# Optimization experiments

Hardware: AMD Instinct MI355X
Metric: run time of the kernel (lower is better)

Reference implementation:

```python
import jax, jax.numpy as jnp
import numpy as np

NEG_SLOPE = 0.2
EPS = 1e-16


def gat_conv(x, src, dst, W, a_src, a_dst, bias, heads, out_ch, n_nodes):
    # x: [N, in], W: [in, heads*out_ch], a_src/a_dst: [heads, out_ch]
    h = (x @ W).reshape(n_nodes, heads, out_ch)            # [N,H,C]
    s_src = jnp.sum(h * a_src[None], axis=-1)              # [N,H]
    s_dst = jnp.sum(h * a_dst[None], axis=-1)              # [N,H]
    e = jax.nn.leaky_relu(s_src[src] + s_dst[dst], NEG_SLOPE)  # [E,H]
    # segment softmax over incoming edges of each destination node
    m = jax.ops.segment_max(e, dst, num_segments=n_nodes)  # [N,H]
    e = jnp.exp(e - m[dst])
    z = jax.ops.segment_sum(e, dst, num_segments=n_nodes)  # [N,H]
    alpha = e / (z[dst] + EPS)                             # [E,H]
    msg = h[src] * alpha[:, :, None]                       # [E,H,C]
    out = jax.ops.segment_sum(msg, dst, num_segments=n_nodes)
    return out.reshape(n_nodes, heads * out_ch) + bias


def setup_inputs() -> dict:
    key = jax.random.key(0)
    ks = jax.random.split(key, 12)
    N, E, D_IN, HID, HEADS, OUT = 100000, 1600000, 16, 128, 8, 3
    C1 = HID // HEADS  # 16 per head
    glorot = lambda k, shape: jax.random.normal(k, shape, jnp.float32) * np.sqrt(2.0 / (shape[0] + shape[-1]))
    return {
        "feature": jax.random.normal(ks[0], (N, D_IN), jnp.float32),
        "edge_index": jax.random.randint(ks[1], (2, E), 0, N, jnp.int64),
        "edge_type": jax.random.randint(ks[2], (E,), 0, 2, jnp.int64),
        "W1": glorot(ks[3], (D_IN, HEADS * C1)),
        "a_src1": glorot(ks[4], (HEADS, C1)),
        "a_dst1": glorot(ks[5], (HEADS, C1)),
        "b1": jnp.zeros((HID,), jnp.float32),
        "W2": glorot(ks[6], (HID, OUT)),
        "a_src2": glorot(ks[7], (1, OUT)),
        "a_dst2": glorot(ks[8], (1, OUT)),
        "b2": jnp.zeros((OUT,), jnp.float32),
    }


def reference(feature, edge_index, edge_type, W1, a_src1, a_dst1, b1, W2, a_src2, a_dst2, b2):
    N = feature.shape[0]
    # PyG GATConv adds self-loops by default
    loop = jnp.arange(N, dtype=edge_index.dtype)
    src = jnp.concatenate([edge_index[0], loop])
    dst = jnp.concatenate([edge_index[1], loop])
    x = gat_conv(feature, src, dst, W1, a_src1, a_dst1, b1, heads=8, out_ch=16, n_nodes=N)
    x = jax.nn.relu(x)
    # dropout is identity in eval mode
    x = gat_conv(x, src, dst, W2, a_src2, a_dst2, b2, heads=1, out_ch=3, n_nodes=N)
    return x
```

## Files before the change

### kernel.cpp

```cpp
#include <hip/hip_runtime.h>
#include <hip/hip_bf16.h>
#include <hip/hip_fp16.h>
#include <math.h>

#define NEG_SLOPE 0.2f
#define GAT_EPS 1e-16f
#define NBMAX 512
#define CAP   6144

__global__ __launch_bounds__(1024) void k_partA(
    const int* __restrict__ ei, int E, int N, int NB, int G2,
    int* __restrict__ cnt, unsigned int* __restrict__ bp,
    const float* __restrict__ x, const float* __restrict__ W1,
    const float* __restrict__ a_src, const float* __restrict__ a_dst,
    __half* __restrict__ h1, float* __restrict__ s_src, float* __restrict__ s_dst)
{
    __shared__ int hist[NBMAX];
    __shared__ int base[NBMAX];
    int t = threadIdx.x;
    if (blockIdx.x >= G2) {
        int gid = (blockIdx.x - G2) * 1024 + t;
        int n = gid >> 5;
        int j4 = gid & 31;
        if (n >= N) return;
        const float4* xr = (const float4*)(x + (size_t)n * 16);
        float4 x0 = xr[0], x1 = xr[1], x2 = xr[2], x3 = xr[3];
        float xs[16] = { x0.x,x0.y,x0.z,x0.w, x1.x,x1.y,x1.z,x1.w,
                         x2.x,x2.y,x2.z,x2.w, x3.x,x3.y,x3.z,x3.w };
        const float4* W4 = (const float4*)W1;
        float4 acc = {0.f, 0.f, 0.f, 0.f};
#pragma unroll
        for (int k = 0; k < 16; ++k) {
            float4 w = W4[k * 32 + j4];
            acc.x += xs[k] * w.x;
            acc.y += xs[k] * w.y;
            acc.z += xs[k] * w.z;
            acc.w += xs[k] * w.w;
        }
        union { __half2 h2v[2]; uint2 u; } pk;
        pk.h2v[0] = __floats2half2_rn(acc.x, acc.y);
        pk.h2v[1] = __floats2half2_rn(acc.z, acc.w);
        ((uint2*)h1)[(size_t)n * 32 + j4] = pk.u;
        float4 av = ((const float4*)a_src)[j4];
        float4 dv = ((const float4*)a_dst)[j4];
        float ps = acc.x*av.x + acc.y*av.y + acc.z*av.z + acc.w*av.w;
        float pd = acc.x*dv.x + acc.y*dv.y + acc.z*dv.z + acc.w*dv.w;
        ps += __shfl_xor(ps, 1); ps += __shfl_xor(ps, 2);
        pd += __shfl_xor(pd, 1); pd += __shfl_xor(pd, 2);
        if ((j4 & 3) == 0) {
            int h = j4 >> 2;
            s_src[n * 8 + h] = ps;
            s_dst[n * 8 + h] = pd;
        }
        return;
    }
    int e0 = blockIdx.x * 4096;
    int srcs[4], dsts[4];
#pragma unroll
    for (int k = 0; k < 4; ++k) {
        int e = e0 + k * 1024 + t;
        if (e < E + N) {
            if (e < E) { srcs[k] = ei[e]; dsts[k] = ei[E + e]; }
            else       { srcs[k] = dsts[k] = e - E; }
        } else dsts[k] = -1;
    }
    if (t < NB) hist[t] = 0;
    __syncthreads();
#pragma unroll
    for (int k = 0; k < 4; ++k)
        if (dsts[k] >= 0) atomicAdd(&hist[dsts[k] >> 8], 1);
    __syncthreads();
    if (t < NB) {
        int c = hist[t];
        base[t] = (c > 0) ? atomicAdd(&cnt[t], c) : 0;
        hist[t] = 0;
    }
    __syncthreads();
#pragma unroll
    for (int k = 0; k < 4; ++k) {
        if (dsts[k] >= 0) {
            int b = dsts[k] >> 8;
            int r = base[b] + atomicAdd(&hist[b], 1);
            if (r < CAP)
                bp[(size_t)b * CAP + r] =
                    ((unsigned)(dsts[k] & 255) << 17) | (unsigned)srcs[k];
        }
    }
}

__global__ __launch_bounds__(512) void k_csr(
    const unsigned int* __restrict__ bp, const int* __restrict__ cnt,
    int* __restrict__ offs, int* __restrict__ ends,
    int* __restrict__ csr, int N)
{
    __shared__ int dcount[256];
    __shared__ int dtmp[256];
    __shared__ int doff[256];
    int b = blockIdx.x;
    int t = threadIdx.x;
    int rb = b * CAP;
    int m = cnt[b]; if (m > CAP) m = CAP;
    if (t < 256) dcount[t] = 0;
    __syncthreads();
    for (int i = t; i < m; i += 512) {
        atomicAdd(&dcount[bp[rb + i] >> 17], 1);
    }
    __syncthreads();
    int v = 0;
    if (t < 256) { v = dcount[t]; dtmp[t] = v; }
    __syncthreads();
    for (int off = 1; off < 256; off <<= 1) {
        int add = (t < 256 && t >= off) ? dtmp[t - off] : 0;
        __syncthreads();
        if (t < 256) dtmp[t] += add;
        __syncthreads();
    }
    if (t < 256) {
        doff[t] = dtmp[t] - v;
        int n = b * 256 + t;
        if (n < N) { offs[n] = rb + doff[t]; ends[n] = rb + dtmp[t]; }
        dcount[t] = 0;
    }
    __syncthreads();
    for (int i = t; i < m; i += 512) {
        unsigned int p = bp[rb + i];
        int dl = p >> 17;
        int r = atomicAdd(&dcount[dl], 1);
        csr[rb + doff[dl] + r] = (int)(p & 0x1FFFFu);
    }
}

__global__ __launch_bounds__(256) void k_agg1(
    const __half* __restrict__ h1, const float* __restrict__ s_src,
    const float* __restrict__ s_dst, const float* __restrict__ b1,
    const float* __restrict__ W2, const float* __restrict__ a_src2,
    const float* __restrict__ a_dst2,
    const int* __restrict__ offs, const int* __restrict__ ends,
    const int* __restrict__ csr_src,
    float4* __restrict__ h2packed, float* __restrict__ s2d, int N)
{
    int gid = blockIdx.x * 256 + threadIdx.x;
    if (gid >= N * 16) return;
    int n = gid >> 4;
    int t = gid & 15;
    int h = t & 7;
    int half = t >> 3;
    int beg = offs[n], end = ends[n];
    float sd = s_dst[n * 8 + h];

    float z = 0.f;
    float acc[16];
#pragma unroll
    for (int c = 0; c < 16; ++c) acc[c] = 0.f;

    union U { float4 f; __half2 hh[4]; };
    int i = beg + half;
    for (; i + 2 < end; i += 4) {
        int sA = csr_src[i];
        int sB = csr_src[i + 2];
        const float4* hA = (const float4*)(h1 + (size_t)sA * 128 + h * 16);
        const float4* hB = (const float4*)(h1 + (size_t)sB * 128 + h * 16);
        U a0, a1, b0, b1v;
        a0.f = hA[0]; a1.f = hA[1];
        b0.f = hB[0]; b1v.f = hB[1];
        float eA = s_src[sA * 8 + h] + sd;
        float eB = s_src[sB * 8 + h] + sd;
        eA = (eA > 0.f) ? eA : NEG_SLOPE * eA;
        eB = (eB > 0.f) ? eB : NEG_SLOPE * eB;
        float pA = __expf(eA);
        float pB = __expf(eB);
        z += pA + pB;
#pragma unroll
        for (int k = 0; k < 4; ++k) {
            float2 vA = __half22float2(a0.hh[k]);
            float2 vB = __half22float2(b0.hh[k]);
            acc[2 * k]     += pA * vA.x + pB * vB.x;
            acc[2 * k + 1] += pA * vA.y + pB * vB.y;
        }
#pragma unroll
        for (int k = 0; k < 4; ++k) {
            float2 vA = __half22float2(a1.hh[k]);
            float2 vB = __half22float2(b1v.hh[k]);
            acc[8 + 2 * k] += pA * vA.x + pB * vB.x;
            acc[9 + 2 * k] += pA * vA.y + pB * vB.y;
        }
    }
    if (i < end) {
        int sA = csr_src[i];
        const float4* hA = (const float4*)(h1 + (size_t)sA * 128 + h * 16);
        U a0, a1;
        a0.f = hA[0]; a1.f = hA[1];
        float eA = s_src[sA * 8 + h] + sd;
        eA = (eA > 0.f) ? eA : NEG_SLOPE * eA;
        float pA = __expf(eA);
        z += pA;
#pragma unroll
        for (int k = 0; k < 4; ++k) {
            float2 vA = __half22float2(a0.hh[k]);
            acc[2 * k]     += pA * vA.x;
            acc[2 * k + 1] += pA * vA.y;
        }
#pragma unroll
        for (int k = 0; k < 4; ++k) {
            float2 vA = __half22float2(a1.hh[k]);
            acc[8 + 2 * k] += pA * vA.x;
            acc[9 + 2 * k] += pA * vA.y;
        }
    }

    z += __shfl_xor(z, 8);
#pragma unroll
    for (int c = 0; c < 16; ++c) acc[c] += __shfl_xor(acc[c], 8);

    float inv = 1.f / (z + GAT_EPS);

    float r0 = 0.f, r1 = 0.f, r2 = 0.f;
    const float* bb = b1 + h * 16;
    const float* w2 = W2 + h * 16 * 3;
#pragma unroll
    for (int c = 0; c < 16; ++c) {
        float xc = fmaxf(acc[c] * inv + bb[c], 0.f);
        r0 += xc * w2[c * 3 + 0];
        r1 += xc * w2[c * 3 + 1];
        r2 += xc * w2[c * 3 + 2];
    }
#pragma unroll
    for (int m = 4; m >= 1; m >>= 1) {
        r0 += __shfl_xor(r0, m);
        r1 += __shfl_xor(r1, m);
        r2 += __shfl_xor(r2, m);
    }
    if (t == 0) {
        float ss = r0 * a_src2[0] + r1 * a_src2[1] + r2 * a_src2[2];
        float dd = r0 * a_dst2[0] + r1 * a_dst2[1] + r2 * a_dst2[2];
        float4 pk = { r0, r1, r2, ss };
        h2packed[n] = pk;
        s2d[n] = dd;
    }
}

__global__ __launch_bounds__(256) void k_agg2(
    const float4* __restrict__ h2packed, const float* __restrict__ s2d,
    const float* __restrict__ b2,
    const int* __restrict__ offs, const int* __restrict__ ends,
    const int* __restrict__ csr_src,
    float* __restrict__ out, int N)
{
    int gid = blockIdx.x * 256 + threadIdx.x;
    if (gid >= N * 8) return;
    int n = gid >> 3;
    int t = gid & 7;
    int beg = offs[n], end = ends[n];
    float sd = s2d[n];
    float z = 0.f, a0 = 0.f, a1 = 0.f, a2 = 0.f;
    for (int i = beg + t; i < end; i += 8) {
        int src = csr_src[i];
        float4 v = h2packed[src];
        float s = v.w + sd;
        s = (s > 0.f) ? s : NEG_SLOPE * s;
        float p = __expf(s);
        z += p;
        a0 += p * v.x; a1 += p * v.y; a2 += p * v.z;
    }
#pragma unroll
    for (int m = 4; m >= 1; m >>= 1) {
        z  += __shfl_xor(z, m);
        a0 += __shfl_xor(a0, m);
        a1 += __shfl_xor(a1, m);
        a2 += __shfl_xor(a2, m);
    }
    if (t == 0) {
        float inv = 1.f / (z + GAT_EPS);
        out[(size_t)n * 3 + 0] = a0 * inv + b2[0];
        out[(size_t)n * 3 + 1] = a1 * inv + b2[1];
        out[(size_t)n * 3 + 2] = a2 * inv + b2[2];
    }
}

extern "C" void kernel_launch(void* const* d_in, const int* in_sizes, int n_in,
                              void* d_out, int out_size, void* d_ws, size_t ws_size,
                              hipStream_t stream)
{
    const float* feature = (const float*)d_in[0];
    const int*   ei      = (const int*)d_in[1];
    const float* W1      = (const float*)d_in[3];
    const float* a_src1  = (const float*)d_in[4];
    const float* a_dst1  = (const float*)d_in[5];
    const float* b1      = (const float*)d_in[6];
    const float* W2      = (const float*)d_in[7];
    const float* a_src2  = (const float*)d_in[8];
    const float* a_dst2  = (const float*)d_in[9];
    const float* b2      = (const float*)d_in[10];

    const int N = in_sizes[0] / 16;
    const int E = in_sizes[1] / 2;
    const int ET = E + N;
    const int NB = (N + 255) >> 8;

    char* p = (char*)d_ws;
    auto alloc = [&](size_t bytes) -> void* {
        void* r = (void*)p;
        p += (bytes + 255) & ~(size_t)255;
        return r;
    };
    __half* h1   = (__half*)alloc((size_t)N * 128 * 2);
    float*  s1s  = (float*)alloc((size_t)N * 8 * 4);
    float*  s1d  = (float*)alloc((size_t)N * 8 * 4);
    float4* h2pk = (float4*)alloc((size_t)N * 16);
    float*  s2dv = (float*)alloc((size_t)N * 4);
    int*    offs = (int*)alloc((size_t)N * 4);
    int*    ends = (int*)alloc((size_t)N * 4);
    int*    csr  = (int*)alloc((size_t)NB * CAP * 4);
    unsigned int* bp = (unsigned int*)alloc((size_t)NB * CAP * 4);
    int*    cnt  = (int*)alloc((size_t)NBMAX * 4);

    hipMemsetAsync(cnt, 0, (size_t)NB * 4, stream);

    int G2 = (ET + 4095) / 4096;
    int G1 = (N * 32 + 1023) / 1024;
    k_partA<<<G2 + G1, 1024, 0, stream>>>(
        ei, E, N, NB, G2, cnt, bp,
        feature, W1, a_src1, a_dst1, h1, s1s, s1d);

    k_csr<<<NB, 512, 0, stream>>>(bp, cnt, offs, ends, csr, N);

    k_agg1<<<(N * 16 + 255) / 256, 256, 0, stream>>>(
        h1, s1s, s1d, b1, W2, a_src2, a_dst2, offs, ends, csr, h2pk, s2dv, N);

    k_agg2<<<(N * 8 + 255) / 256, 256, 0, stream>>>(
        h2pk, s2dv, b2, offs, ends, csr, (float*)d_out, N);
}
```

Before: 172.9 us.

## Store layer-1 features head-major and aggregate one head per block

Layer-1 projected features and attention scores are now stored head-major ([H][N][C]) instead of node-major, and the first aggregation kernel assigns each block a single head over 128 destination nodes. Each block's gathers then touch one 3.2 MB head slice, which is meant to improve L2 locality for the random source gathers. Because the per-node reduction across heads can no longer happen inside a wavefront, per-head partial projections are written to a new N×8 float4 buffer and summed by an extra k_score2 kernel. This adds an extra launch and roughly 12.8 MB of extra write and read traffic.

After: 293.7 us. 1.7x slower.

```diff
diff --git a/kernel.cpp b/kernel.cpp
--- a/kernel.cpp
+++ b/kernel.cpp
@@ -13,7 +13,7 @@
     int* __restrict__ cnt, unsigned int* __restrict__ bp,
     const float* __restrict__ x, const float* __restrict__ W1,
     const float* __restrict__ a_src, const float* __restrict__ a_dst,
-    __half* __restrict__ h1, float* __restrict__ s_src, float* __restrict__ s_dst)
+    __half* __restrict__ h1h, float* __restrict__ s_src_h, float* __restrict__ s_dst_h)
 {
     __shared__ int hist[NBMAX];
     __shared__ int base[NBMAX];
@@ -37,20 +37,20 @@
             acc.z += xs[k] * w.z;
             acc.w += xs[k] * w.w;
         }
+        int h = j4 >> 2, c4 = j4 & 3;
         union { __half2 h2v[2]; uint2 u; } pk;
         pk.h2v[0] = __floats2half2_rn(acc.x, acc.y);
         pk.h2v[1] = __floats2half2_rn(acc.z, acc.w);
-        ((uint2*)h1)[(size_t)n * 32 + j4] = pk.u;
+        ((uint2*)h1h)[((size_t)h * N + n) * 4 + c4] = pk.u;
         float4 av = ((const float4*)a_src)[j4];
         float4 dv = ((const float4*)a_dst)[j4];
         float ps = acc.x*av.x + acc.y*av.y + acc.z*av.z + acc.w*av.w;
         float pd = acc.x*dv.x + acc.y*dv.y + acc.z*dv.z + acc.w*dv.w;
         ps += __shfl_xor(ps, 1); ps += __shfl_xor(ps, 2);
         pd += __shfl_xor(pd, 1); pd += __shfl_xor(pd, 2);
-        if ((j4 & 3) == 0) {
-            int h = j4 >> 2;
-            s_src[n * 8 + h] = ps;
-            s_dst[n * 8 + h] = pd;
+        if (c4 == 0) {
+            s_src_h[(size_t)h * N + n] = ps;
+            s_dst_h[(size_t)h * N + n] = pd;
         }
         return;
     }
@@ -130,23 +130,24 @@
     }
 }
 
-__global__ __launch_bounds__(256) void k_agg1(
-    const __half* __restrict__ h1, const float* __restrict__ s_src,
-    const float* __restrict__ s_dst, const float* __restrict__ b1,
-    const float* __restrict__ W2, const float* __restrict__ a_src2,
-    const float* __restrict__ a_dst2,
+__global__ __launch_bounds__(256) void k_agg1h(
+    const __half* __restrict__ h1h, const float* __restrict__ s_src_h,
+    const float* __restrict__ s_dst_h, const float* __restrict__ b1,
+    const float* __restrict__ W2,
     const int* __restrict__ offs, const int* __restrict__ ends,
     const int* __restrict__ csr_src,
-    float4* __restrict__ h2packed, float* __restrict__ s2d, int N)
-{
-    int gid = blockIdx.x * 256 + threadIdx.x;
-    if (gid >= N * 16) return;
-    int n = gid >> 4;
-    int t = gid & 15;
-    int h = t & 7;
-    int half = t >> 3;
+    float4* __restrict__ h2part, int N)
+{
+    int h = blockIdx.x & 7;
+    int chunk = blockIdx.x >> 3;
+    int t = threadIdx.x;
+    int n = chunk * 128 + (t >> 1);
+    int half = t & 1;
+    if (n >= N) return;
     int beg = offs[n], end = ends[n];
-    float sd = s_dst[n * 8 + h];
+    const float* ssrc = s_src_h + (size_t)h * N;
+    const __half* hbase = h1h + (size_t)h * N * 16;
+    float sd = s_dst_h[(size_t)h * N + n];
 
     float z = 0.f;
     float acc[16];
@@ -158,13 +159,13 @@
     for (; i + 2 < end; i += 4) {
         int sA = csr_src[i];
         int sB = csr_src[i + 2];
-        const float4* hA = (const float4*)(h1 + (size_t)sA * 128 + h * 16);
-        const float4* hB = (const float4*)(h1 + (size_t)sB * 128 + h * 16);
+        const float4* hA = (const float4*)(hbase + (size_t)sA * 16);
+        const float4* hB = (const float4*)(hbase + (size_t)sB * 16);
         U a0, a1, b0, b1v;
         a0.f = hA[0]; a1.f = hA[1];
         b0.f = hB[0]; b1v.f = hB[1];
-        float eA = s_src[sA * 8 + h] + sd;
-        float eB = s_src[sB * 8 + h] + sd;
+        float eA = ssrc[sA] + sd;
+        float eB = ssrc[sB] + sd;
         eA = (eA > 0.f) ? eA : NEG_SLOPE * eA;
         eB = (eB > 0.f) ? eB : NEG_SLOPE * eB;
         float pA = __expf(eA);
@@ -187,10 +188,10 @@
     }
     if (i < end) {
         int sA = csr_src[i];
-        const float4* hA = (const float4*)(h1 + (size_t)sA * 128 + h * 16);
+        const float4* hA = (const float4*)(hbase + (size_t)sA * 16);
         U a0, a1;
         a0.f = hA[0]; a1.f = hA[1];
-        float eA = s_src[sA * 8 + h] + sd;
+        float eA = ssrc[sA] + sd;
         eA = (eA > 0.f) ? eA : NEG_SLOPE * eA;
         float pA = __expf(eA);
         z += pA;
@@ -208,35 +209,45 @@
         }
     }
 
-    z += __shfl_xor(z, 8);
-#pragma unroll
-    for (int c = 0; c < 16; ++c) acc[c] += __shfl_xor(acc[c], 8);
-
-    float inv = 1.f / (z + GAT_EPS);
-
+    z += __shfl_xor(z, 1);
+#pragma unroll
+    for (int c = 0; c < 16; ++c) acc[c] += __shfl_xor(acc[c], 1);
+
+    if (half == 0) {
+        float inv = 1.f / (z + GAT_EPS);
+        float r0 = 0.f, r1 = 0.f, r2 = 0.f;
+        const float* bb = b1 + h * 16;
+        const float* w2 = W2 + h * 16 * 3;
+#pragma unroll
+        for (int c = 0; c < 16; ++c) {
+            float xc = fmaxf(acc[c] * inv + bb[c], 0.f);
+            r0 += xc * w2[c * 3 + 0];
+            r1 += xc * w2[c * 3 + 1];
+            r2 += xc * w2[c * 3 + 2];
+        }
+        float4 pk = { r0, r1, r2, 0.f };
+        h2part[(size_t)h * N + n] = pk;
+    }
+}
+
+__global__ __launch_bounds__(256) void k_score2(
+    const float4* __restrict__ h2part, const float* __restrict__ a_src2,
+    const float* __restrict__ a_dst2,
+    float4* __restrict__ h2pk, float* __restrict__ s2d, int N)
+{
+    int n = blockIdx.x * 256 + threadIdx.x;
+    if (n >= N) return;
     float r0 = 0.f, r1 = 0.f, r2 = 0.f;
-    const float* bb = b1 + h * 16;
-    const float* w2 = W2 + h * 16 * 3;
-#pragma unroll
-    for (int c = 0; c < 16; ++c) {
-        float xc = fmaxf(acc[c] * inv + bb[c], 0.f);
-        r0 += xc * w2[c * 3 + 0];
-        r1 += xc * w2[c * 3 + 1];
-        r2 += xc * w2[c * 3 + 2];
-    }
-#pragma unroll
-    for (int m = 4; m >= 1; m >>= 1) {
-        r0 += __shfl_xor(r0, m);
-        r1 += __shfl_xor(r1, m);
-        r2 += __shfl_xor(r2, m);
-    }
-    if (t == 0) {
-        float ss = r0 * a_src2[0] + r1 * a_src2[1] + r2 * a_src2[2];
-        float dd = r0 * a_dst2[0] + r1 * a_dst2[1] + r2 * a_dst2[2];
-        float4 pk = { r0, r1, r2, ss };
-        h2packed[n] = pk;
-        s2d[n] = dd;
-    }
+#pragma unroll
+    for (int h = 0; h < 8; ++h) {
+        float4 v = h2part[(size_t)h * N + n];
+        r0 += v.x; r1 += v.y; r2 += v.z;
+    }
+    float ss = r0 * a_src2[0] + r1 * a_src2[1] + r2 * a_src2[2];
+    float dd = r0 * a_dst2[0] + r1 * a_dst2[1] + r2 * a_dst2[2];
+    float4 pk = { r0, r1, r2, ss };
+    h2pk[n] = pk;
+    s2d[n] = dd;
 }
 
 __global__ __launch_bounds__(256) void k_agg2(
@@ -303,9 +314,10 @@
         p += (bytes + 255) & ~(size_t)255;
         return r;
     };
-    __half* h1   = (__half*)alloc((size_t)N * 128 * 2);
+    __half* h1h  = (__half*)alloc((size_t)N * 128 * 2);
     float*  s1s  = (float*)alloc((size_t)N * 8 * 4);
     float*  s1d  = (float*)alloc((size_t)N * 8 * 4);
+    float4* h2pt = (float4*)alloc((size_t)N * 8 * 16);
     float4* h2pk = (float4*)alloc((size_t)N * 16);
     float*  s2dv = (float*)alloc((size_t)N * 4);
     int*    offs = (int*)alloc((size_t)N * 4);
@@ -320,12 +332,16 @@
     int G1 = (N * 32 + 1023) / 1024;
     k_partA<<<G2 + G1, 1024, 0, stream>>>(
         ei, E, N, NB, G2, cnt, bp,
-        feature, W1, a_src1, a_dst1, h1, s1s, s1d);
+        feature, W1, a_src1, a_dst1, h1h, s1s, s1d);
 
     k_csr<<<NB, 512, 0, stream>>>(bp, cnt, offs, ends, csr, N);
 
-    k_agg1<<<(N * 16 + 255) / 256, 256, 0, stream>>>(
-        h1, s1s, s1d, b1, W2, a_src2, a_dst2, offs, ends, csr, h2pk, s2dv, N);
+    int chunks = (N + 127) / 128;
+    k_agg1h<<<chunks * 8, 256, 0, stream>>>(
+        h1h, s1s, s1d, b1, W2, offs, ends, csr, h2pt, N);
+
+    k_score2<<<(N + 255) / 256, 256, 0, stream>>>(
+        h2pt, a_src2, a_dst2, h2pk, s2dv, N);
 
     k_agg2<<<(N * 8 + 255) / 256, 256, 0, stream>>>(
         h2pk, s2dv, b2, offs, ends, csr, (float*)d_out, N);
```

## Fuse CSR bucket sort into layer-1 aggregation kernel using shared-memory edge list

Applied to the files above, without the earlier changes.

Merges the per-bucket CSR build and the first-layer attention aggregation into one kernel. Each 1024-thread block sorts its bucket's edges into shared memory and then aggregates its 256 destination nodes straight from that list. The CSR is still written to global memory for the second layer. This removes a launch and the global re-read of the CSR in layer 1, but the fused kernel runs only NB (~391) blocks with 24KB+ of shared memory each, so there may be too few blocks to fill the GPU and latency hiding may suffer.

Result: slower. 185.3 us (+7.2%).

```diff
diff --git a/kernel.cpp b/kernel.cpp
--- a/kernel.cpp
+++ b/kernel.cpp
@@ -88,23 +88,28 @@
     }
 }
 
-__global__ __launch_bounds__(512) void k_csr(
+__global__ __launch_bounds__(1024) void k_agg1b(
+    const __half* __restrict__ h1, const float* __restrict__ s_src,
+    const float* __restrict__ s_dst, const float* __restrict__ b1,
+    const float* __restrict__ W2, const float* __restrict__ a_src2,
+    const float* __restrict__ a_dst2,
     const unsigned int* __restrict__ bp, const int* __restrict__ cnt,
-    int* __restrict__ offs, int* __restrict__ ends,
-    int* __restrict__ csr, int N)
+    int* __restrict__ offs, int* __restrict__ ends, int* __restrict__ csr,
+    float4* __restrict__ h2pk, float* __restrict__ s2d, int N)
 {
     __shared__ int dcount[256];
     __shared__ int dtmp[256];
     __shared__ int doff[256];
+    __shared__ int dlen[256];
+    __shared__ int els[CAP];
     int b = blockIdx.x;
     int t = threadIdx.x;
     int rb = b * CAP;
     int m = cnt[b]; if (m > CAP) m = CAP;
     if (t < 256) dcount[t] = 0;
     __syncthreads();
-    for (int i = t; i < m; i += 512) {
+    for (int i = t; i < m; i += 1024)
         atomicAdd(&dcount[bp[rb + i] >> 17], 1);
-    }
     __syncthreads();
     int v = 0;
     if (t < 256) { v = dcount[t]; dtmp[t] = v; }
@@ -117,125 +122,121 @@
     }
     if (t < 256) {
         doff[t] = dtmp[t] - v;
+        dlen[t] = v;
         int n = b * 256 + t;
-        if (n < N) { offs[n] = rb + doff[t]; ends[n] = rb + dtmp[t]; }
+        if (n < N) { offs[n] = rb + doff[t]; ends[n] = rb + doff[t] + v; }
         dcount[t] = 0;
     }
     __syncthreads();
-    for (int i = t; i < m; i += 512) {
+    for (int i = t; i < m; i += 1024) {
         unsigned int p = bp[rb + i];
         int dl = p >> 17;
         int r = atomicAdd(&dcount[dl], 1);
-        csr[rb + doff[dl] + r] = (int)(p & 0x1FFFFu);
-    }
-}
-
-__global__ __launch_bounds__(256) void k_agg1(
-    const __half* __restrict__ h1, const float* __restrict__ s_src,
-    const float* __restrict__ s_dst, const float* __restrict__ b1,
-    const float* __restrict__ W2, const float* __restrict__ a_src2,
-    const float* __restrict__ a_dst2,
-    const int* __restrict__ offs, const int* __restrict__ ends,
-    const int* __restrict__ csr_src,
-    float4* __restrict__ h2packed, float* __restrict__ s2d, int N)
-{
-    int gid = blockIdx.x * 256 + threadIdx.x;
-    if (gid >= N * 16) return;
-    int n = gid >> 4;
-    int t = gid & 15;
-    int h = t & 7;
-    int half = t >> 3;
-    int beg = offs[n], end = ends[n];
-    float sd = s_dst[n * 8 + h];
-
-    float z = 0.f;
-    float acc[16];
-#pragma unroll
-    for (int c = 0; c < 16; ++c) acc[c] = 0.f;
-
+        int pos = doff[dl] + r;
+        int src = (int)(p & 0x1FFFFu);
+        els[pos] = src;
+        csr[rb + pos] = src;
+    }
+    __syncthreads();
+
+    int tt = t & 15;
+    int h  = tt & 7;
+    int half = tt >> 3;
+    int group = t >> 4;
     union U { float4 f; __half2 hh[4]; };
-    int i = beg + half;
-    for (; i + 2 < end; i += 4) {
-        int sA = csr_src[i];
-        int sB = csr_src[i + 2];
-        const float4* hA = (const float4*)(h1 + (size_t)sA * 128 + h * 16);
-        const float4* hB = (const float4*)(h1 + (size_t)sB * 128 + h * 16);
-        U a0, a1, b0, b1v;
-        a0.f = hA[0]; a1.f = hA[1];
-        b0.f = hB[0]; b1v.f = hB[1];
-        float eA = s_src[sA * 8 + h] + sd;
-        float eB = s_src[sB * 8 + h] + sd;
-        eA = (eA > 0.f) ? eA : NEG_SLOPE * eA;
-        eB = (eB > 0.f) ? eB : NEG_SLOPE * eB;
-        float pA = __expf(eA);
-        float pB = __expf(eB);
-        z += pA + pB;
-#pragma unroll
-        for (int k = 0; k < 4; ++k) {
-            float2 vA = __half22float2(a0.hh[k]);
-            float2 vB = __half22float2(b0.hh[k]);
-            acc[2 * k]     += pA * vA.x + pB * vB.x;
-            acc[2 * k + 1] += pA * vA.y + pB * vB.y;
-        }
-#pragma unroll
-        for (int k = 0; k < 4; ++k) {
-            float2 vA = __half22float2(a1.hh[k]);
-            float2 vB = __half22float2(b1v.hh[k]);
-            acc[8 + 2 * k] += pA * vA.x + pB * vB.x;
-            acc[9 + 2 * k] += pA * vA.y + pB * vB.y;
-        }
-    }
-    if (i < end) {
-        int sA = csr_src[i];
-        const float4* hA = (const float4*)(h1 + (size_t)sA * 128 + h * 16);
-        U a0, a1;
-        a0.f = hA[0]; a1.f = hA[1];
-        float eA = s_src[sA * 8 + h] + sd;
-        eA = (eA > 0.f) ? eA : NEG_SLOPE * eA;
-        float pA = __expf(eA);
-        z += pA;
-#pragma unroll
-        for (int k = 0; k < 4; ++k) {
-            float2 vA = __half22float2(a0.hh[k]);
-            acc[2 * k]     += pA * vA.x;
-            acc[2 * k + 1] += pA * vA.y;
-        }
-#pragma unroll
-        for (int k = 0; k < 4; ++k) {
-            float2 vA = __half22float2(a1.hh[k]);
-            acc[8 + 2 * k] += pA * vA.x;
-            acc[9 + 2 * k] += pA * vA.y;
-        }
-    }
-
-    z += __shfl_xor(z, 8);
-#pragma unroll
-    for (int c = 0; c < 16; ++c) acc[c] += __shfl_xor(acc[c], 8);
-
-    float inv = 1.f / (z + GAT_EPS);
-
-    float r0 = 0.f, r1 = 0.f, r2 = 0.f;
-    const float* bb = b1 + h * 16;
-    const float* w2 = W2 + h * 16 * 3;
-#pragma unroll
-    for (int c = 0; c < 16; ++c) {
-        float xc = fmaxf(acc[c] * inv + bb[c], 0.f);
-        r0 += xc * w2[c * 3 + 0];
-        r1 += xc * w2[c * 3 + 1];
-        r2 += xc * w2[c * 3 + 2];
-    }
-#pragma unroll
-    for (int m = 4; m >= 1; m >>= 1) {
-        r0 += __shfl_xor(r0, m);
-        r1 += __shfl_xor(r1, m);
-        r2 += __shfl_xor(r2, m);
-    }
-    if (t == 0) {
-        float ss = r0 * a_src2[0] + r1 * a_src2[1] + r2 * a_src2[2];
-        float dd = r0 * a_dst2[0] + r1 * a_dst2[1] + r2 * a_dst2[2];
-        float4 pk = { r0, r1, r2, ss };
-        h2packed[n] = pk;
-        s2d[n] = dd;
+#pragma unroll
+    for (int rr = 0; rr < 4; ++rr) {
+        int dl = group + rr * 64;
+        int n = b * 256 + dl;
+        if (n >= N) continue;
+        int beg = doff[dl], end = beg + dlen[dl];
+        float sd = s_dst[n * 8 + h];
+        float z = 0.f;
+        float acc[16];
+#pragma unroll
+        for (int c = 0; c < 16; ++c) acc[c] = 0.f;
+        int i = beg + half;
+        for (; i + 2 < end; i += 4) {
+            int sA = els[i];
+            int sB = els[i + 2];
+            const float4* hA = (const float4*)(h1 + (size_t)sA * 128 + h * 16);
+            const float4* hB = (const float4*)(h1 + (size_t)sB * 128 + h * 16);
+            U a0, a1, b0, b1v;
+            a0.f = hA[0]; a1.f = hA[1];
+            b0.f = hB[0]; b1v.f = hB[1];
+            float eA = s_src[sA * 8 + h] + sd;
+            float eB = s_src[sB * 8 + h] + sd;
+            eA = (eA > 0.f) ? eA : NEG_SLOPE * eA;
+            eB = (eB > 0.f) ? eB : NEG_SLOPE * eB;
+            float pA = __expf(eA);
+            float pB = __expf(eB);
+            z += pA + pB;
+#pragma unroll
+            for (int k = 0; k < 4; ++k) {
+                float2 vA = __half22float2(a0.hh[k]);
+                float2 vB = __half22float2(b0.hh[k]);
+                acc[2 * k]     += pA * vA.x + pB * vB.x;
+                acc[2 * k + 1] += pA * vA.y + pB * vB.y;
+            }
+#pragma unroll
+            for (int k = 0; k < 4; ++k) {
+                float2 vA = __half22float2(a1.hh[k]);
+                float2 vB = __half22float2(b1v.hh[k]);
+                acc[8 + 2 * k] += pA * vA.x + pB * vB.x;
+                acc[9 + 2 * k] += pA * vA.y + pB * vB.y;
+            }
+        }
+        if (i < end) {
+            int sA = els[i];
+            const float4* hA = (const float4*)(h1 + (size_t)sA * 128 + h * 16);
+            U a0, a1;
+            a0.f = hA[0]; a1.f = hA[1];
+            float eA = s_src[sA * 8 + h] + sd;
+            eA = (eA > 0.f) ? eA : NEG_SLOPE * eA;
+            float pA = __expf(eA);
+            z += pA;
+#pragma unroll
+            for (int k = 0; k < 4; ++k) {
+                float2 vA = __half22float2(a0.hh[k]);
+                acc[2 * k]     += pA * vA.x;
+                acc[2 * k + 1] += pA * vA.y;
+            }
+#pragma unroll
+            for (int k = 0; k < 4; ++k) {
+                float2 vA = __half22float2(a1.hh[k]);
+                acc[8 + 2 * k] += pA * vA.x;
+                acc[9 + 2 * k] += pA * vA.y;
+            }
+        }
+
+        z += __shfl_xor(z, 8);
+#pragma unroll
+        for (int c = 0; c < 16; ++c) acc[c] += __shfl_xor(acc[c], 8);
+
+        float inv = 1.f / (z + GAT_EPS);
+        float r0 = 0.f, r1 = 0.f, r2 = 0.f;
+        const float* bb = b1 + h * 16;
+        const float* w2 = W2 + h * 16 * 3;
+#pragma unroll
+        for (int c = 0; c < 16; ++c) {
+            float xc = fmaxf(acc[c] * inv + bb[c], 0.f);
+            r0 += xc * w2[c * 3 + 0];
+            r1 += xc * w2[c * 3 + 1];
+            r2 += xc * w2[c * 3 + 2];
+        }
+#pragma unroll
+        for (int mm = 4; mm >= 1; mm >>= 1) {
+            r0 += __shfl_xor(r0, mm);
+            r1 += __shfl_xor(r1, mm);
+            r2 += __shfl_xor(r2, mm);
+        }
+        if (tt == 0) {
+            float ss = r0 * a_src2[0] + r1 * a_src2[1] + r2 * a_src2[2];
+            float dd = r0 * a_dst2[0] + r1 * a_dst2[1] + r2 * a_dst2[2];
+            float4 pk = { r0, r1, r2, ss };
+            h2pk[n] = pk;
+            s2d[n] = dd;
+        }
     }
 }
 
@@ -322,10 +323,9 @@
         ei, E, N, NB, G2, cnt, bp,
         feature, W1, a_src1, a_dst1, h1, s1s, s1d);
 
-    k_csr<<<NB, 512, 0, stream>>>(bp, cnt, offs, ends, csr, N);
-
-    k_agg1<<<(N * 16 + 255) / 256, 256, 0, stream>>>(
-        h1, s1s, s1d, b1, W2, a_src2, a_dst2, offs, ends, csr, h2pk, s2dv, N);
+    k_agg1b<<<NB, 1024, 0, stream>>>(
+        h1, s1s, s1d, b1, W2, a_src2, a_dst2,
+        bp, cnt, offs, ends, csr, h2pk, s2dv, N);
 
     k_agg2<<<(N * 8 + 255) / 256, 256, 0, stream>>>(
         h2pk, s2dv, b2, offs, ends, csr, (float*)d_out, N);
```
